# Optimization experiments

Measured on AMD Instinct MI355X. Metric: run time of the kernel, lower is better.

The kernel has to match this reference:

```python
import jax, jax.numpy as jnp
import numpy as np

# Dimensions (see init_kwargs): C=out_channels, R=res, PS=pool_size, HN=head_num,
# D=head_dim=R*R//HN, input spatial H=W=PS*R.
B, C, R, PS, HN, D = 16, 512, 32, 3, 8, 128
NORM_C = 0.5


def _avg_pool(x, k):
    b, c, h, w = x.shape
    return x.reshape(b, c, h // k, k, w // k, k).mean(axis=(3, 5))


def _max_pool(x, k):
    b, c, h, w = x.shape
    return x.reshape(b, c, h // k, k, w // k, k).max(axis=(3, 5))


def _to_heads(p):
    # Replicates torch: [B,C,R,R].view(B,R*R,C).permute(0,2,1).view(B,C,HN,D).permute(0,2,1,3)
    t = p.reshape(B, R * R, C).transpose(0, 2, 1)  # [B, C, R*R]
    return t.reshape(B, C, HN, D).transpose(0, 2, 1, 3)  # [B, HN, C, D]


def setup_inputs() -> dict:
    key = jax.random.key(0)
    ks = jax.random.split(key, 6)
    H = PS * R
    x = jax.random.normal(ks[0], (B, C, H, H), jnp.float32)
    # per-head q/k projections (Linear(head_dim, head_dim) per head)
    Wqk = jax.random.normal(ks[1], (HN, D, D), jnp.float32) * (1.0 / np.sqrt(D))
    bqk = jax.random.normal(ks[2], (HN, D), jnp.float32) * 0.01
    # w_p: Linear(C, C) feeding sigmoid gate
    Wp = jax.random.normal(ks[3], (C, C), jnp.float32) * (1.0 / np.sqrt(C))
    bp = jnp.zeros((C,), jnp.float32)
    # w_v: 1x1 Conv2d(C, C)
    Wv = jax.random.normal(ks[4], (C, C), jnp.float32) * (1.0 / np.sqrt(C))
    bv = jax.random.normal(ks[5], (C,), jnp.float32) * 0.01
    return {"x": x, "Wqk": Wqk, "bqk": bqk, "Wp": Wp, "bp": bp,
            "Wv": Wv, "bv": bv, "weight": 0}


def reference(x, Wqk, bqk, Wp, bp, Wv, bv, weight):
    # pooled query / key token grids: [B, C, R, R]
    q_pool = _avg_pool(x, PS)
    k_pool = _max_pool(x, PS)

    # heads over channels: [B, HN, C, D], then per-head linear (torch Linear: y = x W^T + b)
    q = jnp.einsum('bhcd,hed->bhce', _to_heads(q_pool), Wqk) + bqk[None, :, None, :]
    k = jnp.einsum('bhcd,hed->bhce', _to_heads(k_pool), Wqk) + bqk[None, :, None, :]

    # value: 1x1 conv then AvgPool2d(3) -> [B, HN, C, D]
    v_conv = jnp.einsum('bchw,oc->bohw', x, Wv) + bv[None, :, None, None]
    v = _to_heads(_avg_pool(v_conv, 3))

    # channel attention scores: [B, HN, C, C]
    scores = jnp.einsum('bhcd,bhed->bhce', q, k)
    # learned power-law exponent gate: sigmoid(Linear(mean over keys))
    p = jax.nn.sigmoid(scores.mean(axis=-1) @ Wp.T + bp)  # [B, HN, C]
    norm_scores = scores / jnp.power(jnp.float32(D), NORM_C + p[..., None])
    w = jax.nn.softmax(norm_scores, axis=-1)
    attn = jnp.einsum('bhce,bhed->bhcd', w, v)  # [B, HN, C, D]

    # back to [B, R, R, C] (torch permute/view chain)
    attn = attn.transpose(0, 2, 1, 3).reshape(B, C, R * R)
    attn = attn.transpose(0, 2, 1).reshape(B, R, R, C)

    # residual on pooled input (original code's residual shape is inconsistent;
    # we use the pooled token grid, same reshape path as the output)
    resid = q_pool.reshape(B, R * R, C).reshape(B, R, R, C)
    return resid + attn * (1 + weight)
```

## Files before the change

### kernel.cpp

```cpp
#include <hip/hip_runtime.h>
#include <math.h>

typedef unsigned short u16;
typedef short bf16x8 __attribute__((ext_vector_type(8)));
typedef float floatx4 __attribute__((ext_vector_type(4)));
typedef unsigned short ushort4v __attribute__((ext_vector_type(4)));

#define F_QP   0ull
#define F_IPW  8388608ull
#define F_WPT  8454144ull
#define F_END  8716288ull
#define U_QPT_V 0ull
#define U_QPT_P 8388608ull
#define U_KPT_P 16777216ull
#define U_PQ    25165824ull
#define U_PK    33554432ull
#define U_VP    41943040ull
#define U_WV    50331648ull
#define U_WQK   50593792ull

__device__ __forceinline__ u16 f2bf(float f) {
    union { float f; unsigned u; } v; v.f = f;
    return (u16)((v.u + 0x7fffu + ((v.u >> 16) & 1u)) >> 16);
}
__device__ __forceinline__ float bf2f(u16 u) {
    union { unsigned u; float f; } v; v.u = ((unsigned)u) << 16;
    return v.f;
}
__device__ __forceinline__ void ld_async16(const u16* g, u16* l) {
    __builtin_amdgcn_global_load_lds(
        (const __attribute__((address_space(1))) void*)g,
        (__attribute__((address_space(3))) void*)l, 16, 0, 0);
}

__global__ __launch_bounds__(256) void pool_fused(const float* __restrict__ x,
                                                  float* __restrict__ qp,
                                                  u16* __restrict__ qpT_v,
                                                  u16* __restrict__ qpT_p,
                                                  u16* __restrict__ kpT_p) {
    __shared__ __align__(16) float Xs[9216];
    __shared__ float Tq[32][33], Tk[32][33];
    const int tid = threadIdx.x;
    const int i  = blockIdx.x;
    const int c0 = blockIdx.y * 32;
    const int b  = blockIdx.z;
    {
        const float* xb = x + (size_t)b * 4718592 + (size_t)c0 * 9216 + (3 * i) * 96;
        float4* Xs4 = (float4*)Xs;
        #pragma unroll
        for (int it = 0; it < 9; ++it) {
            int f = tid + it * 256;
            int cl = f / 72;
            int rem = f - cl * 72;
            Xs4[f] = *(const float4*)(xb + (size_t)cl * 9216 + rem * 4);
        }
    }
    __syncthreads();
    const int j = tid & 31, cg = tid >> 5;
    #pragma unroll
    for (int p = 0; p < 4; ++p) {
        int cl = p * 8 + cg;
        const float* px = Xs + cl * 288 + 3 * j;
        float s = 0.f, mx = -INFINITY;
        #pragma unroll
        for (int di = 0; di < 3; ++di)
            #pragma unroll
            for (int dj = 0; dj < 3; ++dj) {
                float v = px[di * 96 + dj];
                s += v; mx = fmaxf(mx, v);
            }
        float q = s * (1.f / 9.f);
        Tq[cl][j] = q; Tk[cl][j] = mx;
        qp[(size_t)b * 524288 + (size_t)(c0 + cl) * 1024 + i * 32 + j] = q;
    }
    __syncthreads();
    const int cl = tid & 31, jq = tid >> 5;
    const int rh = i >> 4;
    const int s2 = (c0 + cl) * 2 + rh;
    #pragma unroll
    for (int jj = 0; jj < 4; ++jj) {
        int jw = jq + jj * 8;
        int rr = i * 32 + jw;
        int cc = rr & 511;
        u16 qb = f2bf(Tq[cl][jw]);
        u16 kb = f2bf(Tk[cl][jw]);
        qpT_v[(size_t)b * 524288 + (size_t)rr * 512 + c0 + cl] = qb;
        qpT_p[(size_t)b * 524288 + (size_t)cc * 1024 + s2] = qb;
        kpT_p[(size_t)b * 524288 + (size_t)cc * 1024 + s2] = kb;
    }
}

__global__ __launch_bounds__(256) void prep_w(const float* __restrict__ Wv,
                                              const float* __restrict__ Wqk,
                                              const float* __restrict__ Wp,
                                              u16* __restrict__ Wv_bf,
                                              u16* __restrict__ Wqk_bf,
                                              float* __restrict__ WpT) {
    __shared__ float t[32][33];
    const int blk = blockIdx.x, tid = threadIdx.x;
    if (blk < 384) {
        int i = (blk * 256 + tid) * 4;
        const float* src; u16* dst; int off;
        if (i < 262144) { src = Wv; dst = Wv_bf; off = i; }
        else            { src = Wqk; dst = Wqk_bf; off = i - 262144; }
        float4 v = *(const float4*)(src + off);
        ushort4v o; o.x = f2bf(v.x); o.y = f2bf(v.y); o.z = f2bf(v.z); o.w = f2bf(v.w);
        *(ushort4v*)(dst + off) = o;
    } else {
        int bb = blk - 384;
        int x0 = (bb & 15) * 32, y0 = (bb >> 4) * 32;
        int tx = tid & 31, ty = tid >> 5;
        #pragma unroll
        for (int it = 0; it < 4; ++it)
            t[ty + it * 8][tx] = Wp[(size_t)(y0 + ty + it * 8) * 512 + x0 + tx];
        __syncthreads();
        #pragma unroll
        for (int it = 0; it < 4; ++it)
            WpT[(size_t)(x0 + ty + it * 8) * 512 + y0 + tx] = t[tx][ty + it * 8];
    }
}

__device__ __forceinline__ void gemm_bt_body(const u16* __restrict__ A, int ldA,
                                             const u16* __restrict__ B, int ldB, int K,
                                             u16* As, u16* Bs, floatx4 (&acc)[4][4]) {
    const int tid = threadIdx.x;
    const int lane = tid & 63;
    const int wv = tid >> 6;
    const int wm = (wv & 1) * 64, wn = (wv >> 1) * 64;
    const u16* ga0 = A + (size_t)(tid >> 2) * ldA + (tid & 3) * 8;
    const u16* ga1 = A + (size_t)((tid >> 2) + 64) * ldA + (tid & 3) * 8;
    const u16* gb0 = B + (size_t)(tid >> 2) * ldB + (tid & 3) * 8;
    const u16* gb1 = B + (size_t)((tid >> 2) + 64) * ldB + (tid & 3) * 8;
    u16* la0 = As + tid * 8;
    u16* la1 = As + (tid + 256) * 8;
    u16* lb0 = Bs + tid * 8;
    u16* lb1 = Bs + (tid + 256) * 8;
    const int arow = (lane & 15) * 32 + (lane >> 4) * 8;
    for (int k0 = 0; k0 < K; k0 += 32) {
        ld_async16(ga0 + k0, la0);
        ld_async16(ga1 + k0, la1);
        ld_async16(gb0 + k0, lb0);
        ld_async16(gb1 + k0, lb1);
        __syncthreads();
        bf16x8 af[4], bfr[4];
        #pragma unroll
        for (int i = 0; i < 4; ++i)
            af[i] = *(const bf16x8*)&As[(wm + i * 16) * 32 + arow];
        #pragma unroll
        for (int j = 0; j < 4; ++j)
            bfr[j] = *(const bf16x8*)&Bs[(wn + j * 16) * 32 + arow];
        #pragma unroll
        for (int i = 0; i < 4; ++i)
            #pragma unroll
            for (int j = 0; j < 4; ++j)
                acc[i][j] = __builtin_amdgcn_mfma_f32_16x16x32_bf16(af[i], bfr[j], acc[i][j], 0, 0, 0);
        __syncthreads();
    }
}

__global__ __launch_bounds__(256) void gemms_mfma(const u16* __restrict__ Wv_bf,
                                                  const float* __restrict__ bv,
                                                  const u16* __restrict__ qpT_v,
                                                  u16* __restrict__ vp_bf,
                                                  const u16* __restrict__ qpT_p,
                                                  const u16* __restrict__ kpT_p,
                                                  const u16* __restrict__ Wqk_bf,
                                                  const float* __restrict__ bqk,
                                                  u16* __restrict__ pq_bf,
                                                  u16* __restrict__ pk_bf) {
    __shared__ __align__(16) u16 As[4096], Bs[4096];
    floatx4 acc[4][4] = {};
    const int tid = threadIdx.x, lane = tid & 63, wv = tid >> 6;
    const int wm = (wv & 1) * 64, wn = (wv >> 1) * 64, col = lane & 15, quad = lane >> 4;
    const int blk = blockIdx.x;
    if (blk < 512) {
        const int n0 = (blk & 7) * 128, m0 = ((blk >> 3) & 3) * 128, b = blk >> 5;
        gemm_bt_body(Wv_bf + (size_t)m0 * 512, 512,
                     qpT_v + (size_t)b * 524288 + (size_t)n0 * 512, 512, 512, As, Bs, acc);
        u16* outb = vp_bf + (size_t)b * 524288;
        #pragma unroll
        for (int i = 0; i < 4; ++i)
            #pragma unroll
            for (int r = 0; r < 4; ++r) {
                int m = m0 + wm + i * 16 + quad * 4 + r;
                float bias = bv[m];
                #pragma unroll
                for (int j = 0; j < 4; ++j) {
                    int n = n0 + wn + j * 16 + col;
                    outb[(size_t)m * 1024 + n] = f2bf(acc[i][j][r] + bias);
                }
            }
    } else {
        const int blk2 = blk - 512;
        const int m0 = (blk2 & 3) * 128;
        const int z = blk2 >> 2;
        const int b = z >> 4, h = (z >> 1) & 7, src = z & 1;
        const u16* P = (src ? kpT_p : qpT_p) + (size_t)b * 524288 + (size_t)m0 * 1024 + h * 128;
        gemm_bt_body(P, 1024, Wqk_bf + h * 16384, 128, 128, As, Bs, acc);
        u16* outp = (src ? pk_bf : pq_bf) + (size_t)(b * 8 + h) * 65536 + (size_t)m0 * 128;
        #pragma unroll
        for (int i = 0; i < 4; ++i)
            #pragma unroll
            for (int r = 0; r < 4; ++r) {
                int m = wm + i * 16 + quad * 4 + r;
                #pragma unroll
                for (int j = 0; j < 4; ++j) {
                    int n = wn + j * 16 + col;
                    outp[(size_t)m * 128 + n] = f2bf(acc[i][j][r] + bqk[h * 128 + n]);
                }
            }
    }
}

__global__ __launch_bounds__(256) void gate_fused(const u16* __restrict__ pq_bf,
                                                  const u16* __restrict__ pk_bf,
                                                  const float* __restrict__ WpT,
                                                  const float* __restrict__ bp,
                                                  float* __restrict__ ipw) {
    __shared__ float red[16][128];
    __shared__ float kb[128];
    __shared__ float ms[512];
    const int bh = blockIdx.x, tid = threadIdx.x;
    const u16* pkb = pk_bf + (size_t)bh * 65536;
    const u16* pqb = pq_bf + (size_t)bh * 65536;
    {
        const int dc = tid & 15, rg = tid >> 4;
        float a[8] = {};
        const u16* p = pkb + (size_t)rg * 4096 + dc * 8;
        #pragma unroll 8
        for (int r = 0; r < 32; ++r) {
            bf16x8 v = *(const bf16x8*)(p + (size_t)r * 128);
            #pragma unroll
            for (int k = 0; k < 8; ++k) a[k] += bf2f((u16)v[k]);
        }
        #pragma unroll
        for (int k = 0; k < 8; ++k) red[rg][dc * 8 + k] = a[k];
    }
    __syncthreads();
    if (tid < 128) {
        float s = 0.f;
        #pragma unroll
        for (int g = 0; g < 16; ++g) s += red[g][tid];
        kb[tid] = s * (1.f / 512.f);
    }
    __syncthreads();
    for (int cc = tid; cc < 512; cc += 256) {
        const u16* q = pqb + (size_t)cc * 128;
        float s = 0.f;
        #pragma unroll
        for (int ch = 0; ch < 16; ++ch) {
            bf16x8 v = *(const bf16x8*)(q + ch * 8);
            #pragma unroll
            for (int k = 0; k < 8; ++k) s += bf2f((u16)v[k]) * kb[ch * 8 + k];
        }
        ms[cc] = s;
    }
    __syncthreads();
    {
        const int c2 = tid * 2;
        float a0 = bp[c2], a1 = bp[c2 + 1];
        #pragma unroll 4
        for (int c = 0; c < 512; ++c) {
            float m = ms[c];
            float2 w = *(const float2*)&WpT[(size_t)c * 512 + c2];
            a0 += m * w.x; a1 += m * w.y;
        }
        float p0 = 1.f / (1.f + __expf(-a0));
        float p1 = 1.f / (1.f + __expf(-a1));
        ipw[bh * 512 + c2]     = exp2f(-7.f * (0.5f + p0));
        ipw[bh * 512 + c2 + 1] = exp2f(-7.f * (0.5f + p1));
    }
}

__global__ __launch_bounds__(256, 2) void flash_mfma(const u16* __restrict__ pq_bf,
                                                     const u16* __restrict__ pk_bf,
                                                     const u16* __restrict__ vp_bf,
                                                     const float* __restrict__ ipw,
                                                     const float* __restrict__ qp,
                                                     float* __restrict__ outp,
                                                     const int* __restrict__ wgt) {
    __shared__ __align__(16) u16 As[4096];
    __shared__ __align__(16) u16 Bs[4096];
    __shared__ __align__(16) u16 Et[128 * 136];
    __shared__ float rsS[128];
    __shared__ float ipwS[128];
    const int tid = threadIdx.x, lane = tid & 63, wv = tid >> 6;
    const int wm = (wv & 1) * 64, wn = (wv >> 1) * 64, col = lane & 15, quad = lane >> 4;
    const int bh = blockIdx.y, b = bh >> 3, h = bh & 7;
    const int m0 = blockIdx.x * 128;
    if (tid < 128) { rsS[tid] = 0.f; ipwS[tid] = ipw[bh * 512 + m0 + tid]; }
    const u16* Aq = pq_bf + (size_t)bh * 65536 + (size_t)m0 * 128;
    const u16* Bk = pk_bf + (size_t)bh * 65536;
    const u16* Av = vp_bf + (size_t)b * 524288 + (size_t)h * 65536;
    const int srow = tid >> 2, scol = (tid & 3) * 8;
    u16 *la0 = As + tid * 8, *la1 = As + (tid + 256) * 8;
    u16 *lb0 = Bs + tid * 8, *lb1 = Bs + (tid + 256) * 8;
    const int arow = col * 32 + quad * 8;
    floatx4 accP[4][4] = {};
    __syncthreads();

    for (int n0 = 0; n0 < 512; n0 += 128) {
        floatx4 accS[4][4] = {};
        for (int k0 = 0; k0 < 128; k0 += 32) {
            ld_async16(Aq + (size_t)srow * 128 + k0 + scol, la0);
            ld_async16(Aq + (size_t)(srow + 64) * 128 + k0 + scol, la1);
            ld_async16(Bk + (size_t)(n0 + srow) * 128 + k0 + scol, lb0);
            ld_async16(Bk + (size_t)(n0 + srow + 64) * 128 + k0 + scol, lb1);
            __syncthreads();
            bf16x8 af[4], bfr[4];
            #pragma unroll
            for (int i = 0; i < 4; ++i) af[i] = *(const bf16x8*)&As[(wm + i * 16) * 32 + arow];
            #pragma unroll
            for (int j = 0; j < 4; ++j) bfr[j] = *(const bf16x8*)&Bs[(wn + j * 16) * 32 + arow];
            #pragma unroll
            for (int i = 0; i < 4; ++i)
                #pragma unroll
                for (int j = 0; j < 4; ++j)
                    accS[i][j] = __builtin_amdgcn_mfma_f32_16x16x32_bf16(af[i], bfr[j], accS[i][j], 0, 0, 0);
            __syncthreads();
        }
        #pragma unroll
        for (int i = 0; i < 4; ++i)
            #pragma unroll
            for (int r = 0; r < 4; ++r) {
                int ml = wm + i * 16 + quad * 4 + r;
                float sc = ipwS[ml];
                float p = 0.f;
                #pragma unroll
                for (int j = 0; j < 4; ++j) {
                    float e = __expf(accS[i][j][r] * sc);
                    p += e;
                    Et[ml * 136 + wn + j * 16 + col] = f2bf(e);
                }
                #pragma unroll
                for (int o = 8; o; o >>= 1) p += __shfl_xor(p, o);
                if (col == 0) atomicAdd(&rsS[ml], p);
            }
        __syncthreads();
        for (int k0 = 0; k0 < 128; k0 += 32) {
            ld_async16(Av + (size_t)srow * 512 + n0 + k0 + scol, la0);
            ld_async16(Av + (size_t)(srow + 64) * 512 + n0 + k0 + scol, la1);
            __syncthreads();
            bf16x8 af[4], bfr[4];
            #pragma unroll
            for (int i = 0; i < 4; ++i) af[i] = *(const bf16x8*)&As[(wm + i * 16) * 32 + arow];
            #pragma unroll
            for (int j = 0; j < 4; ++j) bfr[j] = *(const bf16x8*)&Et[(wn + j * 16 + col) * 136 + k0 + quad * 8];
            #pragma unroll
            for (int i = 0; i < 4; ++i)
                #pragma unroll
                for (int j = 0; j < 4; ++j)
                    accP[i][j] = __builtin_amdgcn_mfma_f32_16x16x32_bf16(af[i], bfr[j], accP[i][j], 0, 0, 0);
            __syncthreads();
        }
    }
    const float mult = 1.f + (float)wgt[0];
    #pragma unroll
    for (int j = 0; j < 4; ++j) {
        int nl = wn + j * 16 + col;
        float inv = mult / rsS[nl];
        #pragma unroll
        for (int i = 0; i < 4; ++i)
            #pragma unroll
            for (int r = 0; r < 4; ++r) {
                int d = wm + i * 16 + quad * 4 + r;
                size_t o = (size_t)b * 524288 + (size_t)(h * 128 + d) * 512 + m0 + nl;
                outp[o] = qp[o] + accP[i][j][r] * inv;
            }
    }
}

extern "C" void kernel_launch(void* const* d_in, const int* in_sizes, int n_in,
                              void* d_out, int out_size, void* d_ws, size_t ws_size,
                              hipStream_t stream) {
    const float* x   = (const float*)d_in[0];
    const float* Wqk = (const float*)d_in[1];
    const float* bqk = (const float*)d_in[2];
    const float* Wp  = (const float*)d_in[3];
    const float* bp  = (const float*)d_in[4];
    const float* Wv  = (const float*)d_in[5];
    const float* bv  = (const float*)d_in[6];
    const int*   wgt = (const int*)d_in[7];
    float* out = (float*)d_out;

    float* ws = (float*)d_ws;
    float* qp  = ws + F_QP;
    float* ipw = ws + F_IPW;
    float* WpT = ws + F_WPT;
    u16* ub = (u16*)(ws + F_END);
    u16* qpT_v  = ub + U_QPT_V;
    u16* qpT_p  = ub + U_QPT_P;
    u16* kpT_p  = ub + U_KPT_P;
    u16* pq_bf  = ub + U_PQ;
    u16* pk_bf  = ub + U_PK;
    u16* vp_bf  = ub + U_VP;
    u16* Wv_bf  = ub + U_WV;
    u16* Wqk_bf = ub + U_WQK;

    prep_w<<<640, 256, 0, stream>>>(Wv, Wqk, Wp, Wv_bf, Wqk_bf, WpT);
    pool_fused<<<dim3(32, 16, 16), 256, 0, stream>>>(x, qp, qpT_v, qpT_p, kpT_p);
    gemms_mfma<<<1536, 256, 0, stream>>>(Wv_bf, bv, qpT_v, vp_bf,
                                         qpT_p, kpT_p, Wqk_bf, bqk, pq_bf, pk_bf);
    gate_fused<<<128, 256, 0, stream>>>(pq_bf, pk_bf, WpT, bp, ipw);
    flash_mfma<<<dim3(4, 128), 256, 0, stream>>>(pq_bf, pk_bf, vp_bf, ipw, qp, out, wgt);
}
```

Measured before the change: 582.3 us.

## Merge weight prep into pool kernel, split gate GEMV, restage flash tiles

The weight conversion and Wp transpose blocks are folded into the pooling kernel as extra blocks, which removes one kernel launch. The gate's 512x512 GEMV is split four ways across the channel dimension with a shared-memory reduction, so every thread takes part and each issues wider loads. In the flash kernel the Q fragments are kept in registers for the whole block, and each 128-wide K/V tile is staged once into a larger XOR-swizzled LDS buffer, replacing per-32-slice staging with its many barriers. The cost is higher register use for the Q fragments and more LDS, which may lower occupancy.

```diff
diff --git a/kernel.cpp b/kernel.cpp
--- a/kernel.cpp
+++ b/kernel.cpp
@@ -33,17 +33,48 @@
         (__attribute__((address_space(3))) void*)l, 16, 0, 0);
 }
 
-__global__ __launch_bounds__(256) void pool_fused(const float* __restrict__ x,
-                                                  float* __restrict__ qp,
-                                                  u16* __restrict__ qpT_v,
-                                                  u16* __restrict__ qpT_p,
-                                                  u16* __restrict__ kpT_p) {
+__global__ __launch_bounds__(256) void pool_prep(const float* __restrict__ x,
+                                                 float* __restrict__ qp,
+                                                 u16* __restrict__ qpT_v,
+                                                 u16* __restrict__ qpT_p,
+                                                 u16* __restrict__ kpT_p,
+                                                 const float* __restrict__ Wv,
+                                                 const float* __restrict__ Wqk,
+                                                 const float* __restrict__ Wp,
+                                                 u16* __restrict__ Wv_bf,
+                                                 u16* __restrict__ Wqk_bf,
+                                                 float* __restrict__ WpT) {
     __shared__ __align__(16) float Xs[9216];
     __shared__ float Tq[32][33], Tk[32][33];
     const int tid = threadIdx.x;
-    const int i  = blockIdx.x;
-    const int c0 = blockIdx.y * 32;
-    const int b  = blockIdx.z;
+    const int blk = blockIdx.x;
+    if (blk >= 8192) {
+        const int pb = blk - 8192;
+        if (pb < 384) {
+            int idx = (pb * 256 + tid) * 4;
+            const float* src; u16* dst; int off;
+            if (idx < 262144) { src = Wv; dst = Wv_bf; off = idx; }
+            else              { src = Wqk; dst = Wqk_bf; off = idx - 262144; }
+            float4 v = *(const float4*)(src + off);
+            ushort4v o; o.x = f2bf(v.x); o.y = f2bf(v.y); o.z = f2bf(v.z); o.w = f2bf(v.w);
+            *(ushort4v*)(dst + off) = o;
+        } else {
+            int bb = pb - 384;
+            int x0 = (bb & 15) * 32, y0 = (bb >> 4) * 32;
+            int tx = tid & 31, ty = tid >> 5;
+            #pragma unroll
+            for (int it = 0; it < 4; ++it)
+                Tq[ty + it * 8][tx] = Wp[(size_t)(y0 + ty + it * 8) * 512 + x0 + tx];
+            __syncthreads();
+            #pragma unroll
+            for (int it = 0; it < 4; ++it)
+                WpT[(size_t)(x0 + ty + it * 8) * 512 + y0 + tx] = Tq[tx][ty + it * 8];
+        }
+        return;
+    }
+    const int i  = blk & 31;
+    const int c0 = ((blk >> 5) & 15) * 32;
+    const int b  = blk >> 9;
     {
         const float* xb = x + (size_t)b * 4718592 + (size_t)c0 * 9216 + (3 * i) * 96;
         float4* Xs4 = (float4*)Xs;
@@ -87,36 +118,6 @@
         qpT_v[(size_t)b * 524288 + (size_t)rr * 512 + c0 + cl] = qb;
         qpT_p[(size_t)b * 524288 + (size_t)cc * 1024 + s2] = qb;
         kpT_p[(size_t)b * 524288 + (size_t)cc * 1024 + s2] = kb;
-    }
-}
-
-__global__ __launch_bounds__(256) void prep_w(const float* __restrict__ Wv,
-                                              const float* __restrict__ Wqk,
-                                              const float* __restrict__ Wp,
-                                              u16* __restrict__ Wv_bf,
-                                              u16* __restrict__ Wqk_bf,
-                                              float* __restrict__ WpT) {
-    __shared__ float t[32][33];
-    const int blk = blockIdx.x, tid = threadIdx.x;
-    if (blk < 384) {
-        int i = (blk * 256 + tid) * 4;
-        const float* src; u16* dst; int off;
-        if (i < 262144) { src = Wv; dst = Wv_bf; off = i; }
-        else            { src = Wqk; dst = Wqk_bf; off = i - 262144; }
-        float4 v = *(const float4*)(src + off);
-        ushort4v o; o.x = f2bf(v.x); o.y = f2bf(v.y); o.z = f2bf(v.z); o.w = f2bf(v.w);
-        *(ushort4v*)(dst + off) = o;
-    } else {
-        int bb = blk - 384;
-        int x0 = (bb & 15) * 32, y0 = (bb >> 4) * 32;
-        int tx = tid & 31, ty = tid >> 5;
-        #pragma unroll
-        for (int it = 0; it < 4; ++it)
-            t[ty + it * 8][tx] = Wp[(size_t)(y0 + ty + it * 8) * 512 + x0 + tx];
-        __syncthreads();
-        #pragma unroll
-        for (int it = 0; it < 4; ++it)
-            WpT[(size_t)(x0 + ty + it * 8) * 512 + y0 + tx] = t[tx][ty + it * 8];
     }
 }
 
@@ -220,6 +221,7 @@
     __shared__ float red[16][128];
     __shared__ float kb[128];
     __shared__ float ms[512];
+    __shared__ float part[4][512];
     const int bh = blockIdx.x, tid = threadIdx.x;
     const u16* pkb = pk_bf + (size_t)bh * 65536;
     const u16* pqb = pq_bf + (size_t)bh * 65536;
@@ -257,14 +259,27 @@
     }
     __syncthreads();
     {
+        const int g = tid >> 6, l = tid & 63;
+        const int c2 = l * 8;
+        float a[8] = {};
+        const int cb = g * 128;
+        #pragma unroll 4
+        for (int c = cb; c < cb + 128; ++c) {
+            float m = ms[c];
+            const float* w = WpT + (size_t)c * 512 + c2;
+            float4 w0 = *(const float4*)w;
+            float4 w1 = *(const float4*)(w + 4);
+            a[0] += m * w0.x; a[1] += m * w0.y; a[2] += m * w0.z; a[3] += m * w0.w;
+            a[4] += m * w1.x; a[5] += m * w1.y; a[6] += m * w1.z; a[7] += m * w1.w;
+        }
+        #pragma unroll
+        for (int k = 0; k < 8; ++k) part[g][c2 + k] = a[k];
+    }
+    __syncthreads();
+    {
         const int c2 = tid * 2;
-        float a0 = bp[c2], a1 = bp[c2 + 1];
-        #pragma unroll 4
-        for (int c = 0; c < 512; ++c) {
-            float m = ms[c];
-            float2 w = *(const float2*)&WpT[(size_t)c * 512 + c2];
-            a0 += m * w.x; a1 += m * w.y;
-        }
+        float a0 = bp[c2]     + part[0][c2]     + part[1][c2]     + part[2][c2]     + part[3][c2];
+        float a1 = bp[c2 + 1] + part[0][c2 + 1] + part[1][c2 + 1] + part[2][c2 + 1] + part[3][c2 + 1];
         float p0 = 1.f / (1.f + __expf(-a0));
         float p1 = 1.f / (1.f + __expf(-a1));
         ipw[bh * 512 + c2]     = exp2f(-7.f * (0.5f + p0));
@@ -279,8 +294,7 @@
                                                      const float* __restrict__ qp,
                                                      float* __restrict__ outp,
                                                      const int* __restrict__ wgt) {
-    __shared__ __align__(16) u16 As[4096];
-    __shared__ __align__(16) u16 Bs[4096];
+    __shared__ __align__(16) u16 Stg[16384];
     __shared__ __align__(16) u16 Et[128 * 136];
     __shared__ float rsS[128];
     __shared__ float ipwS[128];
@@ -292,32 +306,36 @@
     const u16* Aq = pq_bf + (size_t)bh * 65536 + (size_t)m0 * 128;
     const u16* Bk = pk_bf + (size_t)bh * 65536;
     const u16* Av = vp_bf + (size_t)b * 524288 + (size_t)h * 65536;
-    const int srow = tid >> 2, scol = (tid & 3) * 8;
-    u16 *la0 = As + tid * 8, *la1 = As + (tid + 256) * 8;
-    u16 *lb0 = Bs + tid * 8, *lb1 = Bs + (tid + 256) * 8;
-    const int arow = col * 32 + quad * 8;
+    bf16x8 afq[4][4];
+    #pragma unroll
+    for (int i = 0; i < 4; ++i)
+        #pragma unroll
+        for (int kk = 0; kk < 4; ++kk)
+            afq[i][kk] = *(const bf16x8*)&Aq[(size_t)(wm + i * 16 + col) * 128 + kk * 32 + quad * 8];
+    const int srow16 = tid >> 4;
+    const int soff = ((((tid & 15) << 4) ^ ((srow16 & 7) << 4)) >> 1);
+    u16* ldst = Stg + tid * 8;
+    const int cswz = (col & 7) << 3;
     floatx4 accP[4][4] = {};
     __syncthreads();
 
     for (int n0 = 0; n0 < 512; n0 += 128) {
+        #pragma unroll
+        for (int it = 0; it < 8; ++it)
+            ld_async16(Bk + (size_t)(n0 + it * 16 + srow16) * 128 + soff, ldst + it * 2048);
+        __syncthreads();
         floatx4 accS[4][4] = {};
-        for (int k0 = 0; k0 < 128; k0 += 32) {
-            ld_async16(Aq + (size_t)srow * 128 + k0 + scol, la0);
-            ld_async16(Aq + (size_t)(srow + 64) * 128 + k0 + scol, la1);
-            ld_async16(Bk + (size_t)(n0 + srow) * 128 + k0 + scol, lb0);
-            ld_async16(Bk + (size_t)(n0 + srow + 64) * 128 + k0 + scol, lb1);
-            __syncthreads();
-            bf16x8 af[4], bfr[4];
-            #pragma unroll
-            for (int i = 0; i < 4; ++i) af[i] = *(const bf16x8*)&As[(wm + i * 16) * 32 + arow];
-            #pragma unroll
-            for (int j = 0; j < 4; ++j) bfr[j] = *(const bf16x8*)&Bs[(wn + j * 16) * 32 + arow];
+        #pragma unroll
+        for (int kk = 0; kk < 4; ++kk) {
+            bf16x8 bfr[4];
+            #pragma unroll
+            for (int j = 0; j < 4; ++j)
+                bfr[j] = *(const bf16x8*)&Stg[(wn + j * 16 + col) * 128 + ((kk * 32 + quad * 8) ^ cswz)];
             #pragma unroll
             for (int i = 0; i < 4; ++i)
                 #pragma unroll
                 for (int j = 0; j < 4; ++j)
-                    accS[i][j] = __builtin_amdgcn_mfma_f32_16x16x32_bf16(af[i], bfr[j], accS[i][j], 0, 0, 0);
-            __syncthreads();
+                    accS[i][j] = __builtin_amdgcn_mfma_f32_16x16x32_bf16(afq[i][kk], bfr[j], accS[i][j], 0, 0, 0);
         }
         #pragma unroll
         for (int i = 0; i < 4; ++i)
@@ -337,22 +355,26 @@
                 if (col == 0) atomicAdd(&rsS[ml], p);
             }
         __syncthreads();
-        for (int k0 = 0; k0 < 128; k0 += 32) {
-            ld_async16(Av + (size_t)srow * 512 + n0 + k0 + scol, la0);
-            ld_async16(Av + (size_t)(srow + 64) * 512 + n0 + k0 + scol, la1);
-            __syncthreads();
-            bf16x8 af[4], bfr[4];
-            #pragma unroll
-            for (int i = 0; i < 4; ++i) af[i] = *(const bf16x8*)&As[(wm + i * 16) * 32 + arow];
-            #pragma unroll
-            for (int j = 0; j < 4; ++j) bfr[j] = *(const bf16x8*)&Et[(wn + j * 16 + col) * 136 + k0 + quad * 8];
+        #pragma unroll
+        for (int it = 0; it < 8; ++it)
+            ld_async16(Av + (size_t)(it * 16 + srow16) * 512 + n0 + soff, ldst + it * 2048);
+        __syncthreads();
+        #pragma unroll
+        for (int kk = 0; kk < 4; ++kk) {
+            bf16x8 av[4], et[4];
             #pragma unroll
             for (int i = 0; i < 4; ++i)
+                av[i] = *(const bf16x8*)&Stg[(wm + i * 16 + col) * 128 + ((kk * 32 + quad * 8) ^ cswz)];
+            #pragma unroll
+            for (int j = 0; j < 4; ++j)
+                et[j] = *(const bf16x8*)&Et[(wn + j * 16 + col) * 136 + kk * 32 + quad * 8];
+            #pragma unroll
+            for (int i = 0; i < 4; ++i)
                 #pragma unroll
                 for (int j = 0; j < 4; ++j)
-                    accP[i][j] = __builtin_amdgcn_mfma_f32_16x16x32_bf16(af[i], bfr[j], accP[i][j], 0, 0, 0);
-            __syncthreads();
-        }
+                    accP[i][j] = __builtin_amdgcn_mfma_f32_16x16x32_bf16(av[i], et[j], accP[i][j], 0, 0, 0);
+        }
+        __syncthreads();
     }
     const float mult = 1.f + (float)wgt[0];
     #pragma unroll
@@ -397,8 +419,8 @@
     u16* Wv_bf  = ub + U_WV;
     u16* Wqk_bf = ub + U_WQK;
 
-    prep_w<<<640, 256, 0, stream>>>(Wv, Wqk, Wp, Wv_bf, Wqk_bf, WpT);
-    pool_fused<<<dim3(32, 16, 16), 256, 0, stream>>>(x, qp, qpT_v, qpT_p, kpT_p);
+    pool_prep<<<8832, 256, 0, stream>>>(x, qp, qpT_v, qpT_p, kpT_p,
+                                        Wv, Wqk, Wp, Wv_bf, Wqk_bf, WpT);
     gemms_mfma<<<1536, 256, 0, stream>>>(Wv_bf, bv, qpT_v, vp_bf,
                                          qpT_p, kpT_p, Wqk_bf, bqk, pq_bf, pk_bf);
     gate_fused<<<128, 256, 0, stream>>>(pq_bf, pk_bf, WpT, bp, ipw);
```

After: 534.1 us. 1.09x faster.
